# Kernel optimization log

Measured on AMD Instinct MI355X. Metric: run time of the kernel, lower is better.

The kernel has to match this reference:

```python
import jax, jax.numpy as jnp
import numpy as np

N_HEADS = 8
N_FEAT = 64
IMG_W = 80
IMG_H = 80
C_DS = 32


def setup_inputs() -> dict:
    key = jax.random.key(0)
    ks = jax.random.split(key, 16)
    n = lambda k, s: jax.random.normal(k, s, dtype=jnp.float32)
    u = lambda k, s: jax.random.uniform(k, s, dtype=jnp.float32)  # torch.rand init
    return {
        # forward args
        "X": n(ks[0], (N_FEAT, IMG_W, IMG_H)),
        "WQ_task": n(ks[1], (N_HEADS, N_FEAT, 1, 1)),
        "BQ_task": n(ks[2], (N_HEADS, N_FEAT, 1, 1)),
        "WK_task": n(ks[3], (N_FEAT, 1, 1)),
        "BK_task": n(ks[4], (N_FEAT, 1, 1)),
        "WV_task": n(ks[5], (C_DS, 1, 1)),
        "BV_task": n(ks[6], (C_DS, 1, 1)),
        # module parameters / buffers
        "WQ_t_minus_1": u(ks[7], (N_HEADS, N_FEAT, 1, 1)),
        "WQ_x": u(ks[8], (1, N_FEAT, 1, 1)),
        "BQ": u(ks[9], (N_HEADS, N_FEAT, 1, 1)),
        "WK_x": u(ks[10], (N_FEAT, 1, 1)),
        "BK": u(ks[11], (N_FEAT, 1, 1)),
        "prev_Q": jnp.zeros((N_HEADS, N_FEAT, IMG_W, IMG_H), jnp.float32),
        "Vconv_w": n(ks[12], (C_DS, N_FEAT, 3, 3)) * 0.05,  # OIHW
        "Vconv_b": n(ks[13], (C_DS,)) * 0.05,
    }


def reference(X, WQ_task, BQ_task, WK_task, BK_task, WV_task, BV_task,
              WQ_t_minus_1, WQ_x, BQ, WK_x, BK, prev_Q, Vconv_w, Vconv_b):
    # Q: (h, f, W, H); K: (f, W, H)
    Q = WQ_task * (WQ_t_minus_1 * prev_Q + WQ_x * X[None] + BQ) + BQ_task
    K = WK_task * (WK_x * X + BK) + BK_task
    # similarity = sum over heads AND features of broadcasted Q*K.
    # Mathematically: sum_{h,f} Q[h,f,a,b] * K[f,c,d] = einsum over head-summed Q.
    Qs = Q.sum(axis=0)                              # (f, W, H)
    sim = jnp.einsum('fab,fcd->abcd', Qs, K)        # (W, H, W, H)
    Wd, Hd = sim.shape[0], sim.shape[1]
    attn = jax.nn.softmax(sim.reshape(Wd, Hd, Wd * Hd), axis=-1)  # (W, H, W*H)
    # V = WV_task * Conv2d(X) + BV_task, flattened over space
    Vc = jax.lax.conv_general_dilated(
        X[None], Vconv_w, window_strides=(1, 1), padding='SAME',
        dimension_numbers=('NCHW', 'OIHW', 'NCHW'))
    Vc = Vc + Vconv_b[None, :, None, None]          # (1, c, W, H)
    V = (WV_task * Vc[0] + BV_task).reshape(C_DS, Wd * Hd)  # (c, W*H)
    # out[c, a, b] = sum_n attn[a, b, n] * V[c, n]
    out = jnp.einsum('abn,cn->cab', attn, V)        # (c, W, H)
    return out
```

## Files before the change

### kernel.cpp

```cpp
#include <hip/hip_runtime.h>
#include <math.h>

#define NPIX  6400
#define NH    8
#define KSPLIT 5
#define KPS   1280
#define KPW   320
#define DITER 5
#define LOG2E 1.4426950408889634f
#define DEFER_THR 11.5f

typedef _Float16 f16x8 __attribute__((ext_vector_type(8)));
typedef __fp16   h16x2 __attribute__((ext_vector_type(2)));
typedef __attribute__((ext_vector_type(16))) float f16v;
typedef __attribute__((ext_vector_type(4)))  float f4v;
typedef __attribute__((ext_vector_type(4)))  int   i4v;
typedef unsigned int u32x2 __attribute__((ext_vector_type(2)));

__device__ __forceinline__ f16v zero16() {
    f16v z = {0,0,0,0,0,0,0,0,0,0,0,0,0,0,0,0};
    return z;
}
__device__ __forceinline__ float exp2fast(float x) {
    float r;
    asm("v_exp_f32 %0, %1" : "=v"(r) : "v"(x));
    return r;
}
__device__ __forceinline__ unsigned pkrtz(float a, float b) {
    h16x2 h = __builtin_amdgcn_cvt_pkrtz(a, b);
    return __builtin_bit_cast(unsigned, h);
}
__device__ __forceinline__ float xhalf_max(float x) {
    unsigned a = __float_as_uint(x), b = a;
    u32x2 r = __builtin_amdgcn_permlane32_swap(a, b, false, false);
    return fmaxf(__uint_as_float(r[0]), __uint_as_float(r[1]));
}
__device__ __forceinline__ float xhalf_sum(float x) {
    unsigned a = __float_as_uint(x), b = a;
    u32x2 r = __builtin_amdgcn_permlane32_swap(a, b, false, false);
    return __uint_as_float(r[0]) + __uint_as_float(r[1]);
}
#define PL32SWAP(a, b) { u32x2 _r = __builtin_amdgcn_permlane32_swap((a), (b), false, false); (a) = _r[0]; (b) = _r[1]; }

__global__ __launch_bounds__(256)
void prep_all(const float* __restrict__ X, const float* __restrict__ prevQ,
              const float* __restrict__ WQ_task, const float* __restrict__ BQ_task,
              const float* __restrict__ WQ_tm1, const float* __restrict__ WQ_x,
              const float* __restrict__ BQ,
              const float* __restrict__ WK_task, const float* __restrict__ BK_task,
              const float* __restrict__ WK_x, const float* __restrict__ BK,
              const float* __restrict__ Wc, const float* __restrict__ bc,
              const float* __restrict__ WV_task, const float* __restrict__ BV_task,
              _Float16* __restrict__ QT, _Float16* __restrict__ KT,
              _Float16* __restrict__ Xp2, _Float16* __restrict__ Wt,
              float* __restrict__ biasV) {
    int bid = blockIdx.x;
    if (bid < 200) {
        int g = bid / 25;
        int p = (bid % 25) * 256 + threadIdx.x;
        f16x8 qv8, kv8;
#pragma unroll
        for (int j = 0; j < 8; ++j) {
            int f = g * 8 + j;
            float x = X[f * NPIX + p];
            float kv = WK_task[f] * (WK_x[f] * x + BK[f]) + BK_task[f];
            float wqx_x = WQ_x[f] * x;
            float a = 0.f;
#pragma unroll
            for (int h = 0; h < NH; ++h) {
                int hf = h * 64 + f;
                float inner = WQ_tm1[hf] * prevQ[hf * NPIX + p] + wqx_x + BQ[hf];
                a += WQ_task[hf] * inner + BQ_task[hf];
            }
            qv8[j] = (_Float16)(a * LOG2E);
            kv8[j] = (_Float16)kv;
        }
        *(f16x8*)(QT + (g * NPIX + p) * 8) = qv8;
        *(f16x8*)(KT + (g * NPIX + p) * 8) = kv8;
    } else if (bid < 227) {
        int idx = (bid - 200) * 256 + threadIdx.x;
        if (idx >= 82 * 82) return;
        int xx = idx / 82, yy = idx % 82;
        _Float16* dst = Xp2 + idx * 64;
        if (xx == 0 || xx == 81 || yy == 0 || yy == 81) {
            f16x8 z = {0, 0, 0, 0, 0, 0, 0, 0};
#pragma unroll
            for (int j = 0; j < 8; ++j) *(f16x8*)(dst + j * 8) = z;
        } else {
            int p = (xx - 1) * 80 + (yy - 1);
#pragma unroll
            for (int j = 0; j < 8; ++j) {
                f16x8 v;
#pragma unroll
                for (int i = 0; i < 8; ++i) v[i] = (_Float16)X[(j * 8 + i) * NPIX + p];
                *(f16x8*)(dst + j * 8) = v;
            }
        }
    } else {
        for (int e = threadIdx.x; e < 9 * 4 * 32 * 16; e += 256) {
            int pos = e / 2048;
            int rem = e - pos * 2048;
            int ft = rem / 512;
            int rem2 = rem - ft * 512;
            int c = rem2 / 16, fi = rem2 - (rem2 / 16) * 16;
            int f = ft * 16 + fi;
            Wt[e] = (_Float16)(WV_task[c] * Wc[c * 576 + f * 9 + pos]);
        }
        if (threadIdx.x < 32)
            biasV[threadIdx.x] = WV_task[threadIdx.x] * bc[threadIdx.x] + BV_task[threadIdx.x];
    }
}

__global__ __launch_bounds__(64)
void conv_mfma(const _Float16* __restrict__ Xp2, const _Float16* __restrict__ Wt,
               const float* __restrict__ biasV, _Float16* __restrict__ VT) {
    const int l = threadIdx.x;
    const int lq = l & 31, h = l >> 5;
    int tile = blockIdx.x;
    int x = tile / 3, y0i = tile % 3;
    int y0 = (y0i == 0) ? 0 : ((y0i == 1) ? 32 : 48);

    f16v o = zero16();
#pragma unroll
    for (int pos = 0; pos < 9; ++pos) {
        int dx = pos / 3, dy = pos % 3;
        const _Float16* xb = Xp2 + ((x + dx) * 82 + (y0 + lq + dy)) * 64 + h * 8;
        const _Float16* wb = Wt + (pos * 4 * 32 + lq) * 16 + h * 8;
#pragma unroll
        for (int ft = 0; ft < 4; ++ft) {
            f16x8 a = *(const f16x8*)(wb + ft * 512);
            f16x8 b = *(const f16x8*)(xb + ft * 16);
            o = __builtin_amdgcn_mfma_f32_32x32x16_f16(a, b, o, 0, 0, 0);
        }
    }
    int p = x * 80 + y0 + lq;
    int vbase = ((p >> 4) * 2 + ((p >> 3) & 1)) * 256 + (p & 7);
#pragma unroll
    for (int r = 0; r < 16; ++r) {
        int c = (r & 3) + 8 * (r >> 2) + 4 * h;
        VT[vbase + c * 8] = (_Float16)(o[r] + biasV[c]);
    }
}

__global__ __launch_bounds__(256, 3)
void attn_mfma(const _Float16* __restrict__ QT,
               const _Float16* __restrict__ KT,
               const _Float16* __restrict__ VT,
               float* __restrict__ PmG, float* __restrict__ PlG,
               _Float16* __restrict__ PaccG) {
    __shared__ __align__(16) char lds[17408];

    const int tid = threadIdx.x;
    const int w = tid >> 6, l = tid & 63;
    const int lq = l & 31, h = l >> 5;
    const int qt = blockIdx.x / KSPLIT, ks = blockIdx.x % KSPLIT;
    const int qbase = qt * 32;
    const int wkbase = ks * KPS + w * KPW;

    f16x8 qf[4];
    {
        const _Float16* qp = QT + (h * NPIX + qbase + lq) * 8;
#pragma unroll
        for (int c = 0; c < 4; ++c) qf[c] = *(const f16x8*)(qp + c * (2 * NPIX * 8));
    }

    const _Float16* kg = KT + (h * NPIX + wkbase + lq) * 8;
    const _Float16* vg = VT + wkbase * 32 + (h * 32 + lq) * 8;

    f16v o = zero16();
    float m = -INFINITY, lsum = 0.f;

    f16x8 kA[2][4], kB[2][4];
#pragma unroll
    for (int i = 0; i < 4; ++i) {
        kA[0][i] = *(const f16x8*)(kg + i * (2 * NPIX * 8));
        kB[0][i] = *(const f16x8*)(kg + i * (2 * NPIX * 8) + 256);
    }

#pragma unroll
    for (int it = 0; it < DITER; ++it) {
        const int cur = it & 1, nxt = cur ^ 1;

        f16x8 vA0 = *(const f16x8*)(vg +    0);
        f16x8 vA1 = *(const f16x8*)(vg +  512);
        f16x8 vB0 = *(const f16x8*)(vg + 1024);
        f16x8 vB1 = *(const f16x8*)(vg + 1536);
        vg += 2048;

        if (it + 1 < DITER) {
            kg += 512;
#pragma unroll
            for (int i = 0; i < 4; ++i) {
                kA[nxt][i] = *(const f16x8*)(kg + i * (2 * NPIX * 8));
                kB[nxt][i] = *(const f16x8*)(kg + i * (2 * NPIX * 8) + 256);
            }
        }

        f16v sA = zero16(), sB = zero16();
#pragma unroll
        for (int i = 0; i < 4; ++i) {
            sA = __builtin_amdgcn_mfma_f32_32x32x16_f16(kA[cur][i], qf[i], sA, 0, 0, 0);
            sB = __builtin_amdgcn_mfma_f32_32x32x16_f16(kB[cur][i], qf[i], sB, 0, 0, 0);
        }

        float t8[8];
#pragma unroll
        for (int r = 0; r < 8; ++r)
            t8[r] = fmaxf(fmaxf(sA[2 * r], sA[2 * r + 1]),
                          fmaxf(sB[2 * r], sB[2 * r + 1]));
        float mx = fmaxf(fmaxf(fmaxf(t8[0], t8[1]), fmaxf(t8[2], t8[3])),
                         fmaxf(fmaxf(t8[4], t8[5]), fmaxf(t8[6], t8[7])));
        mx = xhalf_max(mx);
        if (__any(mx > m + DEFER_THR)) {
            float mn = fmaxf(m, mx);
            float sc = exp2fast(m - mn);
            lsum *= sc;
#pragma unroll
            for (int r = 0; r < 16; ++r) o[r] *= sc;
            m = mn;
        }
#pragma unroll
        for (int r = 0; r < 16; ++r) sA[r] = exp2fast(sA[r] - m);
#pragma unroll
        for (int r = 0; r < 16; ++r) sB[r] = exp2fast(sB[r] - m);
        float ps = 0.f;
#pragma unroll
        for (int r = 0; r < 16; ++r) ps += sA[r] + sB[r];
        lsum += xhalf_sum(ps);

        {
            unsigned p0 = pkrtz(sA[0],  sA[1]),  p1 = pkrtz(sA[2],  sA[3]);
            unsigned p2 = pkrtz(sA[4],  sA[5]),  p3 = pkrtz(sA[6],  sA[7]);
            unsigned p4 = pkrtz(sA[8],  sA[9]),  p5 = pkrtz(sA[10], sA[11]);
            unsigned p6 = pkrtz(sA[12], sA[13]), p7 = pkrtz(sA[14], sA[15]);
            PL32SWAP(p0, p2); PL32SWAP(p1, p3); PL32SWAP(p4, p6); PL32SWAP(p5, p7);
            i4v f0 = { (int)p0, (int)p1, (int)p2, (int)p3 };
            i4v f1 = { (int)p4, (int)p5, (int)p6, (int)p7 };
            o = __builtin_amdgcn_mfma_f32_32x32x16_f16(vA0, __builtin_bit_cast(f16x8, f0), o, 0, 0, 0);
            o = __builtin_amdgcn_mfma_f32_32x32x16_f16(vA1, __builtin_bit_cast(f16x8, f1), o, 0, 0, 0);
        }
        {
            unsigned p0 = pkrtz(sB[0],  sB[1]),  p1 = pkrtz(sB[2],  sB[3]);
            unsigned p2 = pkrtz(sB[4],  sB[5]),  p3 = pkrtz(sB[6],  sB[7]);
            unsigned p4 = pkrtz(sB[8],  sB[9]),  p5 = pkrtz(sB[10], sB[11]);
            unsigned p6 = pkrtz(sB[12], sB[13]), p7 = pkrtz(sB[14], sB[15]);
            PL32SWAP(p0, p2); PL32SWAP(p1, p3); PL32SWAP(p4, p6); PL32SWAP(p5, p7);
            i4v f0 = { (int)p0, (int)p1, (int)p2, (int)p3 };
            i4v f1 = { (int)p4, (int)p5, (int)p6, (int)p7 };
            o = __builtin_amdgcn_mfma_f32_32x32x16_f16(vB0, __builtin_bit_cast(f16x8, f0), o, 0, 0, 0);
            o = __builtin_amdgcn_mfma_f32_32x32x16_f16(vB1, __builtin_bit_cast(f16x8, f1), o, 0, 0, 0);
        }
    }

    float* mm = (float*)(lds + 16384);
    float* ll = (float*)(lds + 16896);
#pragma unroll
    for (int rg = 0; rg < 4; ++rg) {
        f4v val = { o[rg * 4 + 0], o[rg * 4 + 1], o[rg * 4 + 2], o[rg * 4 + 3] };
        int cb = rg * 8 + 4 * h;
        int byte = (w * 32 + lq) * 128 + ((cb * 4) ^ ((lq & 7) << 4));
        *(f4v*)(lds + byte) = val;
    }
    if (l < 32) { mm[w * 32 + lq] = m; ll[w * 32 + lq] = lsum; }
    __syncthreads();

    {
        int q = tid >> 3, cb = (tid & 7) * 4;
        float m0 = mm[q], m1 = mm[32 + q], m2 = mm[64 + q], m3 = mm[96 + q];
        float M = fmaxf(fmaxf(m0, m1), fmaxf(m2, m3));
        float e0 = exp2fast(m0 - M), e1 = exp2fast(m1 - M);
        float e2 = exp2fast(m2 - M), e3 = exp2fast(m3 - M);
        float L = ll[q] * e0 + ll[32 + q] * e1 + ll[64 + q] * e2 + ll[96 + q] * e3;
        float rL = 1.f / L;
        int swz = (q & 7) << 4;
        f4v a0 = *(f4v*)(lds + (0 * 32 + q) * 128 + ((cb * 4) ^ swz));
        f4v a1 = *(f4v*)(lds + (1 * 32 + q) * 128 + ((cb * 4) ^ swz));
        f4v a2 = *(f4v*)(lds + (2 * 32 + q) * 128 + ((cb * 4) ^ swz));
        f4v a3 = *(f4v*)(lds + (3 * 32 + q) * 128 + ((cb * 4) ^ swz));
        int qg = qbase + q;
        _Float16 outp[4];
        outp[0] = (_Float16)((a0[0] * e0 + a1[0] * e1 + a2[0] * e2 + a3[0] * e3) * rL);
        outp[1] = (_Float16)((a0[1] * e0 + a1[1] * e1 + a2[1] * e2 + a3[1] * e3) * rL);
        outp[2] = (_Float16)((a0[2] * e0 + a1[2] * e1 + a2[2] * e2 + a3[2] * e3) * rL);
        outp[3] = (_Float16)((a0[3] * e0 + a1[3] * e1 + a2[3] * e2 + a3[3] * e3) * rL);
        *(unsigned long long*)(PaccG + ks * 204800 + qg * 32 + cb) =
            *(unsigned long long*)outp;
        if ((tid & 7) == 0) { PmG[ks * NPIX + qg] = M; PlG[ks * NPIX + qg] = L; }
    }
}

__global__ __launch_bounds__(256)
void merge_out(const float* __restrict__ Pm, const float* __restrict__ Pl,
               const _Float16* __restrict__ Pacc, float* __restrict__ out) {
    int idx = blockIdx.x * 256 + threadIdx.x;
    int q = idx >> 5, c = idx & 31;
    float mv[KSPLIT];
    float M = -INFINITY;
#pragma unroll
    for (int ksi = 0; ksi < KSPLIT; ++ksi) { mv[ksi] = Pm[ksi * NPIX + q]; M = fmaxf(M, mv[ksi]); }
    float den = 0.f, num = 0.f;
#pragma unroll
    for (int ksi = 0; ksi < KSPLIT; ++ksi) {
        float wgt = Pl[ksi * NPIX + q] * exp2fast(mv[ksi] - M);
        den += wgt;
        num += (float)Pacc[ksi * 204800 + q * 32 + c] * wgt;
    }
    out[c * NPIX + q] = num / den;
}

extern "C" void kernel_launch(void* const* d_in, const int* in_sizes, int n_in,
                              void* d_out, int out_size, void* d_ws, size_t ws_size,
                              hipStream_t stream) {
    const float* X       = (const float*)d_in[0];
    const float* WQ_task = (const float*)d_in[1];
    const float* BQ_task = (const float*)d_in[2];
    const float* WK_task = (const float*)d_in[3];
    const float* BK_task = (const float*)d_in[4];
    const float* WV_task = (const float*)d_in[5];
    const float* BV_task = (const float*)d_in[6];
    const float* WQ_tm1  = (const float*)d_in[7];
    const float* WQ_x    = (const float*)d_in[8];
    const float* BQ      = (const float*)d_in[9];
    const float* WK_x    = (const float*)d_in[10];
    const float* BK      = (const float*)d_in[11];
    const float* prev_Q  = (const float*)d_in[12];
    const float* Vconv_w = (const float*)d_in[13];
    const float* Vconv_b = (const float*)d_in[14];

    char* wsb = (char*)d_ws;
    _Float16* QT    = (_Float16*)(wsb + 0);
    _Float16* KT    = (_Float16*)(wsb + 819200);
    _Float16* VT    = (_Float16*)(wsb + 1638400);
    _Float16* Xp2   = (_Float16*)(wsb + 2048000);
    _Float16* Wt    = (_Float16*)(wsb + 2909184);
    float*    biasV = (float*)(wsb + 2946048);
    float*    PmG   = (float*)(wsb + 2946176);
    float*    PlG   = (float*)(wsb + 3074176);
    _Float16* PaccG = (_Float16*)(wsb + 3202176);

    prep_all<<<228, 256, 0, stream>>>(X, prev_Q, WQ_task, BQ_task, WQ_tm1, WQ_x, BQ,
                                      WK_task, BK_task, WK_x, BK,
                                      Vconv_w, Vconv_b, WV_task, BV_task,
                                      QT, KT, Xp2, Wt, biasV);
    conv_mfma<<<240, 64, 0, stream>>>(Xp2, Wt, biasV, VT);
    attn_mfma<<<200 * KSPLIT, 256, 0, stream>>>(QT, KT, VT, PmG, PlG, PaccG);
    merge_out<<<800, 256, 0, stream>>>(PmG, PlG, PaccG, (float*)d_out);
}
```

Before: 41.23 us.

## Split prep Q/K work across more blocks and raise attention occupancy

```diff
diff --git a/kernel.cpp b/kernel.cpp
--- a/kernel.cpp
+++ b/kernel.cpp
@@ -11,6 +11,7 @@
 #define DEFER_THR 11.5f
 
 typedef _Float16 f16x8 __attribute__((ext_vector_type(8)));
+typedef _Float16 f16x4 __attribute__((ext_vector_type(4)));
 typedef __fp16   h16x2 __attribute__((ext_vector_type(2)));
 typedef __attribute__((ext_vector_type(16))) float f16v;
 typedef __attribute__((ext_vector_type(4)))  float f4v;
@@ -55,13 +56,14 @@
               _Float16* __restrict__ Xp2, _Float16* __restrict__ Wt,
               float* __restrict__ biasV) {
     int bid = blockIdx.x;
-    if (bid < 200) {
-        int g = bid / 25;
-        int p = (bid % 25) * 256 + threadIdx.x;
-        f16x8 qv8, kv8;
-#pragma unroll
-        for (int j = 0; j < 8; ++j) {
-            int f = g * 8 + j;
+    if (bid < 400) {
+        int f0 = (bid / 25) * 4;
+        int p  = (bid % 25) * 256 + threadIdx.x;
+        int g  = f0 >> 3;
+        f16x4 qv4, kv4;
+#pragma unroll
+        for (int j = 0; j < 4; ++j) {
+            int f = f0 + j;
             float x = X[f * NPIX + p];
             float kv = WK_task[f] * (WK_x[f] * x + BK[f]) + BK_task[f];
             float wqx_x = WQ_x[f] * x;
@@ -72,13 +74,13 @@
                 float inner = WQ_tm1[hf] * prevQ[hf * NPIX + p] + wqx_x + BQ[hf];
                 a += WQ_task[hf] * inner + BQ_task[hf];
             }
-            qv8[j] = (_Float16)(a * LOG2E);
-            kv8[j] = (_Float16)kv;
-        }
-        *(f16x8*)(QT + (g * NPIX + p) * 8) = qv8;
-        *(f16x8*)(KT + (g * NPIX + p) * 8) = kv8;
-    } else if (bid < 227) {
-        int idx = (bid - 200) * 256 + threadIdx.x;
+            qv4[j] = (_Float16)(a * LOG2E);
+            kv4[j] = (_Float16)kv;
+        }
+        *(f16x4*)(QT + (g * NPIX + p) * 8 + (f0 & 7)) = qv4;
+        *(f16x4*)(KT + (g * NPIX + p) * 8 + (f0 & 7)) = kv4;
+    } else if (bid < 427) {
+        int idx = (bid - 400) * 256 + threadIdx.x;
         if (idx >= 82 * 82) return;
         int xx = idx / 82, yy = idx % 82;
         _Float16* dst = Xp2 + idx * 64;
@@ -142,7 +144,7 @@
     }
 }
 
-__global__ __launch_bounds__(256, 3)
+__global__ __launch_bounds__(256, 4)
 void attn_mfma(const _Float16* __restrict__ QT,
                const _Float16* __restrict__ KT,
                const _Float16* __restrict__ VT,
@@ -170,38 +172,31 @@
     f16v o = zero16();
     float m = -INFINITY, lsum = 0.f;
 
-    f16x8 kA[2][4], kB[2][4];
-#pragma unroll
-    for (int i = 0; i < 4; ++i) {
-        kA[0][i] = *(const f16x8*)(kg + i * (2 * NPIX * 8));
-        kB[0][i] = *(const f16x8*)(kg + i * (2 * NPIX * 8) + 256);
-    }
-
 #pragma unroll
     for (int it = 0; it < DITER; ++it) {
-        const int cur = it & 1, nxt = cur ^ 1;
-
+        f16x8 kA0 = *(const f16x8*)(kg + 0 * (2 * NPIX * 8));
+        f16x8 kA1 = *(const f16x8*)(kg + 1 * (2 * NPIX * 8));
+        f16x8 kA2 = *(const f16x8*)(kg + 2 * (2 * NPIX * 8));
+        f16x8 kA3 = *(const f16x8*)(kg + 3 * (2 * NPIX * 8));
+        f16x8 kB0 = *(const f16x8*)(kg + 0 * (2 * NPIX * 8) + 256);
+        f16x8 kB1 = *(const f16x8*)(kg + 1 * (2 * NPIX * 8) + 256);
+        f16x8 kB2 = *(const f16x8*)(kg + 2 * (2 * NPIX * 8) + 256);
+        f16x8 kB3 = *(const f16x8*)(kg + 3 * (2 * NPIX * 8) + 256);
         f16x8 vA0 = *(const f16x8*)(vg +    0);
         f16x8 vA1 = *(const f16x8*)(vg +  512);
         f16x8 vB0 = *(const f16x8*)(vg + 1024);
         f16x8 vB1 = *(const f16x8*)(vg + 1536);
-        vg += 2048;
-
-        if (it + 1 < DITER) {
-            kg += 512;
-#pragma unroll
-            for (int i = 0; i < 4; ++i) {
-                kA[nxt][i] = *(const f16x8*)(kg + i * (2 * NPIX * 8));
-                kB[nxt][i] = *(const f16x8*)(kg + i * (2 * NPIX * 8) + 256);
-            }
-        }
+        kg += 512; vg += 2048;
 
         f16v sA = zero16(), sB = zero16();
-#pragma unroll
-        for (int i = 0; i < 4; ++i) {
-            sA = __builtin_amdgcn_mfma_f32_32x32x16_f16(kA[cur][i], qf[i], sA, 0, 0, 0);
-            sB = __builtin_amdgcn_mfma_f32_32x32x16_f16(kB[cur][i], qf[i], sB, 0, 0, 0);
-        }
+        sA = __builtin_amdgcn_mfma_f32_32x32x16_f16(kA0, qf[0], sA, 0, 0, 0);
+        sB = __builtin_amdgcn_mfma_f32_32x32x16_f16(kB0, qf[0], sB, 0, 0, 0);
+        sA = __builtin_amdgcn_mfma_f32_32x32x16_f16(kA1, qf[1], sA, 0, 0, 0);
+        sB = __builtin_amdgcn_mfma_f32_32x32x16_f16(kB1, qf[1], sB, 0, 0, 0);
+        sA = __builtin_amdgcn_mfma_f32_32x32x16_f16(kA2, qf[2], sA, 0, 0, 0);
+        sB = __builtin_amdgcn_mfma_f32_32x32x16_f16(kB2, qf[2], sB, 0, 0, 0);
+        sA = __builtin_amdgcn_mfma_f32_32x32x16_f16(kA3, qf[3], sA, 0, 0, 0);
+        sB = __builtin_amdgcn_mfma_f32_32x32x16_f16(kB3, qf[3], sB, 0, 0, 0);
 
         float t8[8];
 #pragma unroll
@@ -338,7 +333,7 @@
     float*    PlG   = (float*)(wsb + 3074176);
     _Float16* PaccG = (_Float16*)(wsb + 3202176);
 
-    prep_all<<<228, 256, 0, stream>>>(X, prev_Q, WQ_task, BQ_task, WQ_tm1, WQ_x, BQ,
+    prep_all<<<428, 256, 0, stream>>>(X, prev_Q, WQ_task, BQ_task, WQ_tm1, WQ_x, BQ,
                                       WK_task, BK_task, WK_x, BK,
                                       Vconv_w, Vconv_b, WV_task, BV_task,
                                       QT, KT, Xp2, Wt, biasV);
```

New measurement: 48.68 us. +18.1%, slower.
